# Performance work log

Measured on AMD Instinct MI355X. Metric: run time of the kernel, lower is better.

## Reference

```python
import jax, jax.numpy as jnp
import numpy as np

G, N, E, C = 4, 50000, 800000, 128


def setup_inputs() -> dict:
    key = jax.random.key(0)
    ks = jax.random.split(key, 8)
    x = jax.random.normal(ks[0], (G, N, C), dtype=jnp.float32)
    edge_index = jax.random.randint(ks[1], (G, 2, E), 0, N, dtype=jnp.int64)
    s = 1.0 / np.sqrt(C)
    W1 = jax.random.normal(ks[2], (G, C, C), dtype=jnp.float32) * s
    W2 = jax.random.normal(ks[3], (G, C, C), dtype=jnp.float32) * s
    W3 = jax.random.normal(ks[4], (G, C, C), dtype=jnp.float32) * s
    b1 = jnp.zeros((G, C), dtype=jnp.float32)
    b2 = jnp.zeros((G, C), dtype=jnp.float32)
    b3 = jnp.zeros((G, C), dtype=jnp.float32)
    return {"x": x, "edge_index": edge_index, "W1": W1, "b1": b1,
            "W2": W2, "b2": b2, "W3": W3, "b3": b3}


def _gcn_layer(x, src, dst, deg_inv_sqrt, W, b):
    # PyG GCNConv: linear, then D^-1/2 (A+I) D^-1/2 aggregation, then bias.
    h = x @ W                                   # [N, C_out]
    norm = deg_inv_sqrt[src] * deg_inv_sqrt[dst]  # [E+N]
    msg = h[src] * norm[:, None]                # gather + scale
    out = jax.ops.segment_sum(msg, dst, num_segments=x.shape[0])
    return out + b


def _forward_one(x, ei, W1, b1, W2, b2, W3, b3):
    n = x.shape[0]
    loops = jnp.arange(n, dtype=ei.dtype)
    src = jnp.concatenate([ei[0], loops])       # add self-loops
    dst = jnp.concatenate([ei[1], loops])
    deg = jax.ops.segment_sum(jnp.ones_like(src, dtype=x.dtype), dst, num_segments=n)
    dis = jnp.where(deg > 0, jax.lax.rsqrt(deg), 0.0)
    x = _gcn_layer(x, src, dst, dis, W1, b1)
    x = _gcn_layer(x, src, dst, dis, W2, b2)
    x = _gcn_layer(x, src, dst, dis, W3, b3)
    return x


def reference(x, edge_index, W1, b1, W2, b2, W3, b3):
    # vmap over the num_graphs independent GCN stacks, then concat node dim
    out = jax.vmap(_forward_one)(x, edge_index, W1, b1, W2, b2, W3, b3)
    return out.reshape(-1, out.shape[-1])       # [G*N, out_channels]
```

## Files before the change

kernel.cpp:

```cpp
#include <hip/hip_runtime.h>

#define NG 4
#define NN 50000
#define NE 800000
#define NC 128
#define NB 196
#define NBT (NG * NB)
#define CAPB 48
#define LBS (NB + 1)

typedef _Float16 half8 __attribute__((ext_vector_type(8)));
typedef _Float16 half4 __attribute__((ext_vector_type(4)));
typedef float f32x4 __attribute__((ext_vector_type(4)));

__global__ __launch_bounds__(256) void zero_kernel(int* __restrict__ a, int n) {
  int i = blockIdx.x * blockDim.x + threadIdx.x;
  if (i < n) a[i] = 0;
}

__global__ __launch_bounds__(256) void bucket_count(
    const int* __restrict__ ei, int* __restrict__ bktCnt) {
  __shared__ int lcnt[NB];
  int g = blockIdx.y;
  for (int i = threadIdx.x; i < NB; i += 256) lcnt[i] = 0;
  __syncthreads();
  const int* dstp = ei + (size_t)g * 2 * NE + NE;
  int e0 = blockIdx.x * 16384;
  for (int t = threadIdx.x; t < 16384; t += 256) {
    int e = e0 + t;
    if (e < NE) atomicAdd(&lcnt[dstp[e] >> 8], 1);
  }
  __syncthreads();
  for (int i = threadIdx.x; i < NB; i += 256)
    if (lcnt[i]) atomicAdd(&bktCnt[g * NB + i], lcnt[i]);
}

__global__ __launch_bounds__(1024) void scan_buckets(
    const int* __restrict__ bktCnt, int* __restrict__ bktBase,
    int* __restrict__ bktCur) {
  __shared__ int wsum[16];
  int tid = threadIdx.x, lane = tid & 63, wv = tid >> 6;
  int v = (tid < NBT) ? bktCnt[tid] : 0;
  int incl = v;
  #pragma unroll
  for (int d2 = 1; d2 < 64; d2 <<= 1) {
    int t = __shfl_up(incl, d2, 64);
    if (lane >= d2) incl += t;
  }
  if (lane == 63) wsum[wv] = incl;
  __syncthreads();
  if (tid == 0) {
    int s = 0;
    #pragma unroll
    for (int w = 0; w < 16; ++w) { int t = wsum[w]; wsum[w] = s; s += t; }
  }
  __syncthreads();
  int excl = wsum[wv] + incl - v;
  if (tid <= NBT) bktBase[tid] = excl;
  if (tid < NBT) bktCur[tid] = excl;
}

__global__ __launch_bounds__(256) void bucket_scatter(
    const int* __restrict__ ei, int* __restrict__ bktCur,
    unsigned int* __restrict__ rec) {
  __shared__ int lcnt[NB];
  __shared__ int lbase[NB];
  __shared__ unsigned int lbin[CAPB * LBS];
  int g = blockIdx.y;
  int tid = threadIdx.x;
  for (int i = tid; i < NB; i += 256) lcnt[i] = 0;
  __syncthreads();
  const int* srcp = ei + (size_t)g * 2 * NE;
  const int* dstp = srcp + NE;
  int e0 = blockIdx.x * 4096;
  for (int t = tid; t < 4096; t += 256) {
    int e = e0 + t;
    if (e < NE) {
      int s = srcp[e], d = dstp[e];
      int b = d >> 8;
      unsigned int r = ((unsigned int)(d & 255) << 16) | (unsigned int)s;
      int pos = atomicAdd(&lcnt[b], 1);
      if (pos < CAPB) lbin[pos * LBS + b] = r;
      else { int gp = atomicAdd(&bktCur[g * NB + b], 1); rec[gp] = r; }
    }
  }
  __syncthreads();
  if (tid < NB) {
    int n = lcnt[tid]; if (n > CAPB) n = CAPB;
    lbase[tid] = n ? atomicAdd(&bktCur[g * NB + tid], n) : 0;
  }
  __syncthreads();
  int lane = tid & 63, wv = tid >> 6;
  for (int b = wv; b < NB; b += 4) {
    int n = lcnt[b]; if (n > CAPB) n = CAPB;
    if (lane < n) rec[lbase[b] + lane] = lbin[lane * LBS + b];
  }
}

__global__ __launch_bounds__(256) void build_csr(
    const unsigned int* __restrict__ rec, const int* __restrict__ bktBase,
    unsigned short* __restrict__ col, int* __restrict__ off,
    float* __restrict__ dis) {
  __shared__ int cnt[256];
  __shared__ int offv[256];
  __shared__ int cnt2[256];
  __shared__ int wsum[4];
  int g = blockIdx.y, b = blockIdx.x;
  int idx = g * NB + b;
  int rb = bktBase[idx], re = bktBase[idx + 1];
  int tid = threadIdx.x;
  cnt[tid] = 0;
  __syncthreads();
  for (int j = rb + tid; j < re; j += 256)
    atomicAdd(&cnt[(rec[j] >> 16) & 255], 1);
  __syncthreads();
  int lane = tid & 63, wv = tid >> 6;
  int v = cnt[tid], incl = v;
  #pragma unroll
  for (int d2 = 1; d2 < 64; d2 <<= 1) {
    int t = __shfl_up(incl, d2, 64);
    if (lane >= d2) incl += t;
  }
  if (lane == 63) wsum[wv] = incl;
  __syncthreads();
  if (tid == 0) {
    int s = 0;
    #pragma unroll
    for (int w = 0; w < 4; ++w) { int t = wsum[w]; wsum[w] = s; s += t; }
  }
  __syncthreads();
  int excl = wsum[wv] + incl - v;
  offv[tid] = excl;
  cnt2[tid] = 0;
  int node = b * 256 + tid;
  if (node < NN) {
    off[g * (NN + 1) + node] = rb + excl;
    dis[(size_t)g * NN + node] = rsqrtf((float)(v + 1));
  }
  if (b == NB - 1 && tid == 0) off[g * (NN + 1) + NN] = re;
  __syncthreads();
  for (int j = rb + tid; j < re; j += 256) {
    unsigned int r = rec[j];
    int dl = (r >> 16) & 255;
    int p = rb + offv[dl] + atomicAdd(&cnt2[dl], 1);
    col[p] = (unsigned short)(r & 0xFFFF);
  }
}

__global__ __launch_bounds__(256) void gemm_mfma_kernel(
    const float* __restrict__ x, const float* __restrict__ W,
    const float* __restrict__ dis, _Float16* __restrict__ h) {
  __shared__ _Float16 Wt[2][128 * 128];
  int g = blockIdx.y;
  int row0 = blockIdx.x * 128;
  int tid = threadIdx.x;
  int lane = tid & 63;
  int wv = tid >> 6;
  int kc = lane >> 4;
  int lr = lane & 15;
  const float* Wg = W + (size_t)g * NC * NC;
  const float* xg = x + (size_t)g * NN * NC;

  {
    int n = tid & 127;
    int kq = (tid >> 7) & 1;
    #pragma unroll
    for (int iter = 0; iter < 16; ++iter) {
      int k4 = iter * 8 + kq * 4;
      float w0 = Wg[(size_t)(k4 + 0) * NC + n];
      float w1 = Wg[(size_t)(k4 + 1) * NC + n];
      float w2 = Wg[(size_t)(k4 + 2) * NC + n];
      float w3 = Wg[(size_t)(k4 + 3) * NC + n];
      half4 hi, lo;
      hi[0] = (_Float16)w0; lo[0] = (_Float16)(w0 - (float)hi[0]);
      hi[1] = (_Float16)w1; lo[1] = (_Float16)(w1 - (float)hi[1]);
      hi[2] = (_Float16)w2; lo[2] = (_Float16)(w2 - (float)hi[2]);
      hi[3] = (_Float16)w3; lo[3] = (_Float16)(w3 - (float)hi[3]);
      int base = n * 128 + ((iter ^ (n & 15)) << 3) + kq * 4;
      *(half4*)&Wt[0][base] = hi;
      *(half4*)&Wt[1][base] = lo;
    }
  }
  __syncthreads();

  f32x4 acc[2][8];
  #pragma unroll
  for (int mb = 0; mb < 2; ++mb)
    #pragma unroll
    for (int nb = 0; nb < 8; ++nb)
      acc[mb][nb] = (f32x4){0.f, 0.f, 0.f, 0.f};

  for (int kstep = 0; kstep < 4; ++kstep) {
    half8 ah[2], al[2];
    #pragma unroll
    for (int mb = 0; mb < 2; ++mb) {
      int row = row0 + wv * 32 + mb * 16 + lr;
      if (row > NN - 1) row = NN - 1;
      const float* xp = xg + (size_t)row * NC + kstep * 32 + kc * 8;
      float4 v0 = *(const float4*)xp;
      float4 v1 = *(const float4*)(xp + 4);
      float vv0 = v0.x, vv1 = v0.y, vv2 = v0.z, vv3 = v0.w;
      float vv4 = v1.x, vv5 = v1.y, vv6 = v1.z, vv7 = v1.w;
      _Float16 t;
      t = (_Float16)vv0; ah[mb][0] = t; al[mb][0] = (_Float16)(vv0 - (float)t);
      t = (_Float16)vv1; ah[mb][1] = t; al[mb][1] = (_Float16)(vv1 - (float)t);
      t = (_Float16)vv2; ah[mb][2] = t; al[mb][2] = (_Float16)(vv2 - (float)t);
      t = (_Float16)vv3; ah[mb][3] = t; al[mb][3] = (_Float16)(vv3 - (float)t);
      t = (_Float16)vv4; ah[mb][4] = t; al[mb][4] = (_Float16)(vv4 - (float)t);
      t = (_Float16)vv5; ah[mb][5] = t; al[mb][5] = (_Float16)(vv5 - (float)t);
      t = (_Float16)vv6; ah[mb][6] = t; al[mb][6] = (_Float16)(vv6 - (float)t);
      t = (_Float16)vv7; ah[mb][7] = t; al[mb][7] = (_Float16)(vv7 - (float)t);
    }
    #pragma unroll
    for (int nb = 0; nb < 8; ++nb) {
      int n = nb * 16 + lr;
      int chunk = kstep * 4 + kc;
      int boff = n * 128 + ((chunk ^ (n & 15)) << 3);
      half8 bh = *(const half8*)&Wt[0][boff];
      half8 bl = *(const half8*)&Wt[1][boff];
      #pragma unroll
      for (int mb = 0; mb < 2; ++mb) {
        acc[mb][nb] = __builtin_amdgcn_mfma_f32_16x16x32_f16(ah[mb], bh, acc[mb][nb], 0, 0, 0);
        acc[mb][nb] = __builtin_amdgcn_mfma_f32_16x16x32_f16(al[mb], bh, acc[mb][nb], 0, 0, 0);
        acc[mb][nb] = __builtin_amdgcn_mfma_f32_16x16x32_f16(ah[mb], bl, acc[mb][nb], 0, 0, 0);
      }
    }
  }

  const float* disg = dis + (size_t)g * NN;
  _Float16* hg = h + (size_t)g * NN * NC;
  #pragma unroll
  for (int mb = 0; mb < 2; ++mb) {
    #pragma unroll
    for (int reg = 0; reg < 4; ++reg) {
      int row = row0 + wv * 32 + mb * 16 + kc * 4 + reg;
      if (row < NN) {
        float dsc = disg[row];
        half8 o;
        #pragma unroll
        for (int nb = 0; nb < 8; ++nb)
          o[nb] = (_Float16)(acc[mb][nb][reg] * dsc);
        *(half8*)(hg + (size_t)row * NC + lr * 8) = o;
      }
    }
  }
}

__global__ __launch_bounds__(256) void agg_kernel(
    const _Float16* __restrict__ h, const int* __restrict__ off,
    const unsigned short* __restrict__ col, const float* __restrict__ dis,
    const float* __restrict__ b, float* __restrict__ out) {
  int g = blockIdx.y;
  int node = blockIdx.x * 16 + (threadIdx.x >> 4);
  if (node >= NN) return;
  int l = threadIdx.x & 15;
  const half8* h8 = (const half8*)(h + (size_t)g * NN * NC);
  float a0[8], a1[8], a2[8], a3[8];
  half8 v = h8[(size_t)node * 16 + l];
  #pragma unroll
  for (int i = 0; i < 8; ++i) {
    a0[i] = (float)v[i]; a1[i] = 0.f; a2[i] = 0.f; a3[i] = 0.f;
  }
  int s = off[g * (NN + 1) + node];
  int e = off[g * (NN + 1) + node + 1];
  int j = s;
  for (; j + 4 <= e; j += 4) {
    int c0 = col[j], c1 = col[j + 1], c2 = col[j + 2], c3 = col[j + 3];
    half8 v0 = h8[(size_t)c0 * 16 + l];
    half8 v1 = h8[(size_t)c1 * 16 + l];
    half8 v2 = h8[(size_t)c2 * 16 + l];
    half8 v3 = h8[(size_t)c3 * 16 + l];
    #pragma unroll
    for (int i = 0; i < 8; ++i) {
      a0[i] += (float)v0[i]; a1[i] += (float)v1[i];
      a2[i] += (float)v2[i]; a3[i] += (float)v3[i];
    }
  }
  for (; j < e; ++j) {
    half8 vr = h8[(size_t)col[j] * 16 + l];
    #pragma unroll
    for (int i = 0; i < 8; ++i) a0[i] += (float)vr[i];
  }
  float dn = dis[g * NN + node];
  float* og = out + ((size_t)g * NN + node) * NC;
  const float* bg = b + (size_t)g * NC;
  #pragma unroll
  for (int i = 0; i < 8; ++i) {
    float val = (a0[i] + a1[i] + a2[i] + a3[i]) * dn + bg[i * 16 + l];
    og[i * 16 + l] = val;
  }
}

extern "C" void kernel_launch(void* const* d_in, const int* in_sizes, int n_in,
                              void* d_out, int out_size, void* d_ws, size_t ws_size,
                              hipStream_t stream) {
  const float* x  = (const float*)d_in[0];
  const int*   ei = (const int*)d_in[1];
  const float* W1 = (const float*)d_in[2];
  const float* b1 = (const float*)d_in[3];
  const float* W2 = (const float*)d_in[4];
  const float* b2 = (const float*)d_in[5];
  const float* W3 = (const float*)d_in[6];
  const float* b3 = (const float*)d_in[7];
  float* out = (float*)d_out;

  char* ws = (char*)d_ws;
  size_t p = 0;
  auto carve = [&](size_t bytes) -> char* {
    char* r = ws + p;
    p += (bytes + 255) & ~(size_t)255;
    return r;
  };
  int*            bktCnt  = (int*)           carve((size_t)NBT * 4);
  int*            bktBase = (int*)           carve((size_t)(NBT + 1) * 4);
  int*            bktCur  = (int*)           carve((size_t)NBT * 4);
  unsigned int*   rec     = (unsigned int*)  carve((size_t)NG * NE * 4);
  unsigned short* col     = (unsigned short*)carve((size_t)NG * NE * 2);
  int*            off     = (int*)           carve((size_t)NG * (NN + 1) * 4);
  float*          dis     = (float*)         carve((size_t)NG * NN * 4);
  _Float16*       hbuf    = (_Float16*)      carve((size_t)NG * NN * NC * 2);

  zero_kernel<<<(NBT + 255) / 256, 256, 0, stream>>>(bktCnt, NBT);
  bucket_count<<<dim3((NE + 16383) / 16384, NG), 256, 0, stream>>>(ei, bktCnt);
  scan_buckets<<<1, 1024, 0, stream>>>(bktCnt, bktBase, bktCur);
  bucket_scatter<<<dim3((NE + 4095) / 4096, NG), 256, 0, stream>>>(ei, bktCur, rec);
  build_csr<<<dim3(NB, NG), 256, 0, stream>>>(rec, bktBase, col, off, dis);

  dim3 ggrid((NN + 127) / 128, NG);
  dim3 agrid((NN + 15) / 16, NG);

  gemm_mfma_kernel<<<ggrid, 256, 0, stream>>>(x, W1, dis, hbuf);
  agg_kernel<<<agrid, 256, 0, stream>>>(hbuf, off, col, dis, b1, out);
  gemm_mfma_kernel<<<ggrid, 256, 0, stream>>>(out, W2, dis, hbuf);
  agg_kernel<<<agrid, 256, 0, stream>>>(hbuf, off, col, dis, b2, out);
  gemm_mfma_kernel<<<ggrid, 256, 0, stream>>>(out, W3, dis, hbuf);
  agg_kernel<<<agrid, 256, 0, stream>>>(hbuf, off, col, dis, b3, out);
}
```

Baseline: 531.4 us.

## Split aggregation across channel quarters per graph and un-permute GEMM output layout

The aggregation kernel now runs once per graph, and each block handles one 32-channel quarter of 16 nodes with half2 loads. Block ids are interleaved so that neighbouring blocks cover the same nodes in different quarters, which is meant to improve cache locality when gathering h rows. The GEMM now writes h in natural column order instead of the previously permuted order, and uses a new LDS swizzle key to match. The trade-off is narrower per-lane gathers, four times as many column-index and offset reads, and four times as many kernel launches.

```diff
diff --git a/kernel.cpp b/kernel.cpp
--- a/kernel.cpp
+++ b/kernel.cpp
@@ -11,6 +11,7 @@
 
 typedef _Float16 half8 __attribute__((ext_vector_type(8)));
 typedef _Float16 half4 __attribute__((ext_vector_type(4)));
+typedef _Float16 half2_t __attribute__((ext_vector_type(2)));
 typedef float f32x4 __attribute__((ext_vector_type(4)));
 
 __global__ __launch_bounds__(256) void zero_kernel(int* __restrict__ a, int n) {
@@ -164,6 +165,7 @@
   {
     int n = tid & 127;
     int kq = (tid >> 7) & 1;
+    int key = ((n >> 3) ^ n) & 7;
     #pragma unroll
     for (int iter = 0; iter < 16; ++iter) {
       int k4 = iter * 8 + kq * 4;
@@ -176,7 +178,7 @@
       hi[1] = (_Float16)w1; lo[1] = (_Float16)(w1 - (float)hi[1]);
       hi[2] = (_Float16)w2; lo[2] = (_Float16)(w2 - (float)hi[2]);
       hi[3] = (_Float16)w3; lo[3] = (_Float16)(w3 - (float)hi[3]);
-      int base = n * 128 + ((iter ^ (n & 15)) << 3) + kq * 4;
+      int base = n * 128 + ((iter ^ key) << 3) + kq * 4;
       *(half4*)&Wt[0][base] = hi;
       *(half4*)&Wt[1][base] = lo;
     }
@@ -213,9 +215,10 @@
     }
     #pragma unroll
     for (int nb = 0; nb < 8; ++nb) {
-      int n = nb * 16 + lr;
+      int n = lr * 8 + nb;
+      int key = ((n >> 3) ^ n) & 7;
       int chunk = kstep * 4 + kc;
-      int boff = n * 128 + ((chunk ^ (n & 15)) << 3);
+      int boff = n * 128 + ((chunk ^ key) << 3);
       half8 bh = *(const half8*)&Wt[0][boff];
       half8 bl = *(const half8*)&Wt[1][boff];
       #pragma unroll
@@ -249,46 +252,43 @@
 __global__ __launch_bounds__(256) void agg_kernel(
     const _Float16* __restrict__ h, const int* __restrict__ off,
     const unsigned short* __restrict__ col, const float* __restrict__ dis,
-    const float* __restrict__ b, float* __restrict__ out) {
-  int g = blockIdx.y;
-  int node = blockIdx.x * 16 + (threadIdx.x >> 4);
+    const float* __restrict__ b, float* __restrict__ out, int g) {
+  int bid = blockIdx.x;
+  int q = (bid >> 1) & 3;
+  int chunk = ((bid >> 3) << 1) | (bid & 1);
+  int node = chunk * 16 + (threadIdx.x >> 4);
   if (node >= NN) return;
   int l = threadIdx.x & 15;
-  const half8* h8 = (const half8*)(h + (size_t)g * NN * NC);
-  float a0[8], a1[8], a2[8], a3[8];
-  half8 v = h8[(size_t)node * 16 + l];
-  #pragma unroll
-  for (int i = 0; i < 8; ++i) {
-    a0[i] = (float)v[i]; a1[i] = 0.f; a2[i] = 0.f; a3[i] = 0.f;
-  }
+  int co = q * 32 + l * 2;
+  const _Float16* hg = h + (size_t)g * NN * NC + co;
+  half2_t v = *(const half2_t*)(hg + (size_t)node * NC);
+  float ax0 = (float)v[0], ay0 = (float)v[1];
+  float ax1 = 0.f, ay1 = 0.f, ax2 = 0.f, ay2 = 0.f, ax3 = 0.f, ay3 = 0.f;
   int s = off[g * (NN + 1) + node];
   int e = off[g * (NN + 1) + node + 1];
   int j = s;
   for (; j + 4 <= e; j += 4) {
     int c0 = col[j], c1 = col[j + 1], c2 = col[j + 2], c3 = col[j + 3];
-    half8 v0 = h8[(size_t)c0 * 16 + l];
-    half8 v1 = h8[(size_t)c1 * 16 + l];
-    half8 v2 = h8[(size_t)c2 * 16 + l];
-    half8 v3 = h8[(size_t)c3 * 16 + l];
-    #pragma unroll
-    for (int i = 0; i < 8; ++i) {
-      a0[i] += (float)v0[i]; a1[i] += (float)v1[i];
-      a2[i] += (float)v2[i]; a3[i] += (float)v3[i];
-    }
+    half2_t v0 = *(const half2_t*)(hg + (size_t)c0 * NC);
+    half2_t v1 = *(const half2_t*)(hg + (size_t)c1 * NC);
+    half2_t v2 = *(const half2_t*)(hg + (size_t)c2 * NC);
+    half2_t v3 = *(const half2_t*)(hg + (size_t)c3 * NC);
+    ax0 = fmaf((float)v0[0], 1.f, ax0); ay0 = fmaf((float)v0[1], 1.f, ay0);
+    ax1 = fmaf((float)v1[0], 1.f, ax1); ay1 = fmaf((float)v1[1], 1.f, ay1);
+    ax2 = fmaf((float)v2[0], 1.f, ax2); ay2 = fmaf((float)v2[1], 1.f, ay2);
+    ax3 = fmaf((float)v3[0], 1.f, ax3); ay3 = fmaf((float)v3[1], 1.f, ay3);
   }
   for (; j < e; ++j) {
-    half8 vr = h8[(size_t)col[j] * 16 + l];
-    #pragma unroll
-    for (int i = 0; i < 8; ++i) a0[i] += (float)vr[i];
+    half2_t vr = *(const half2_t*)(hg + (size_t)col[j] * NC);
+    ax0 = fmaf((float)vr[0], 1.f, ax0); ay0 = fmaf((float)vr[1], 1.f, ay0);
   }
   float dn = dis[g * NN + node];
-  float* og = out + ((size_t)g * NN + node) * NC;
-  const float* bg = b + (size_t)g * NC;
-  #pragma unroll
-  for (int i = 0; i < 8; ++i) {
-    float val = (a0[i] + a1[i] + a2[i] + a3[i]) * dn + bg[i * 16 + l];
-    og[i * 16 + l] = val;
-  }
+  float bx = b[(size_t)g * NC + co];
+  float by = b[(size_t)g * NC + co + 1];
+  float2 o;
+  o.x = (ax0 + ax1 + ax2 + ax3) * dn + bx;
+  o.y = (ay0 + ay1 + ay2 + ay3) * dn + by;
+  *(float2*)(out + ((size_t)g * NN + node) * NC + co) = o;
 }
 
 extern "C" void kernel_launch(void* const* d_in, const int* in_sizes, int n_in,
@@ -327,12 +327,15 @@
   build_csr<<<dim3(NB, NG), 256, 0, stream>>>(rec, bktBase, col, off, dis);
 
   dim3 ggrid((NN + 127) / 128, NG);
-  dim3 agrid((NN + 15) / 16, NG);
+  int  agrid = 1563 * 8;
 
   gemm_mfma_kernel<<<ggrid, 256, 0, stream>>>(x, W1, dis, hbuf);
-  agg_kernel<<<agrid, 256, 0, stream>>>(hbuf, off, col, dis, b1, out);
+  for (int g = 0; g < NG; ++g)
+    agg_kernel<<<agrid, 256, 0, stream>>>(hbuf, off, col, dis, b1, out, g);
   gemm_mfma_kernel<<<ggrid, 256, 0, stream>>>(out, W2, dis, hbuf);
-  agg_kernel<<<agrid, 256, 0, stream>>>(hbuf, off, col, dis, b2, out);
+  for (int g = 0; g < NG; ++g)
+    agg_kernel<<<agrid, 256, 0, stream>>>(hbuf, off, col, dis, b2, out, g);
   gemm_mfma_kernel<<<ggrid, 256, 0, stream>>>(out, W3, dis, hbuf);
-  agg_kernel<<<agrid, 256, 0, stream>>>(hbuf, off, col, dis, b3, out);
-}
+  for (int g = 0; g < NG; ++g)
+    agg_kernel<<<agrid, 256, 0, stream>>>(hbuf, off, col, dis, b3, out, g);
+}
```

Result: slower. 803.4 us (+51.2%).
